# Kernel optimization log

Hardware: AMD Instinct MI355X
Metric: run time of the kernel (lower is better)

## Reference

```python
import jax, jax.numpy as jnp
import numpy as np

N = 4096
F = 256
E = 65536
NEG = -1e30  # mask value for non-neighbors in distance top-k


def setup_inputs() -> dict:
    key = jax.random.key(0)
    k1, k2, k3, k4, k5 = jax.random.split(key, 5)
    edge_index = jax.random.randint(k1, (2, E), 0, N)
    edge_weight = jax.random.uniform(k2, (E,), dtype=jnp.float32)
    features = jax.random.normal(k3, (N, F), dtype=jnp.float32)
    theta_1 = jax.random.uniform(k4, (1,), dtype=jnp.float32)
    theta_2 = jax.random.uniform(k5, (1,), dtype=jnp.float32)
    return {"edge_index": edge_index, "edge_weight": edge_weight,
            "features": features, "theta_1": theta_1, "theta_2": theta_2}


def reference(edge_index, edge_weight, features, theta_1, theta_2):
    n = features.shape[0]
    row, col = edge_index[0], edge_index[1]
    # Adjacency construction is done on detached numpy in the original.
    w = jax.lax.stop_gradient(edge_weight)
    X = jax.lax.stop_gradient(features)
    # sp.csr_matrix sums duplicate (i,j) entries -> scatter-add; + I; clamp >1 to 1
    A = jnp.zeros((n, n), jnp.float32).at[row, col].add(w)
    A = A + jnp.eye(n, dtype=jnp.float32)
    A = jnp.where(A > 1.0, 1.0, A)
    A2 = A @ A  # adjs[1] = sp_A ** 2
    # generate_sparse_ids mutates both A and A_robust(=A2 for r=2) with setdiag(0)
    off = 1.0 - jnp.eye(n, dtype=jnp.float32)
    A = A * off
    A2 = A2 * off
    D = jnp.sum(A != 0.0, axis=1)    # per-node degree (count_nonzero)
    Dr = jnp.sum(A2 != 0.0, axis=1)  # robust (2-hop) degree
    Df = D.astype(jnp.float32)
    d_thres = jnp.mean(Df) + 2.0 * jnp.std(Df)  # euclidean metric branch
    # squared-euclidean distances via gram trick: ||xu - xv||^2
    sq = jnp.sum(X * X, axis=1)
    dist2 = sq[:, None] + sq[None, :] - 2.0 * (X @ X.T)
    nbr2 = A2 != 0.0  # A_robust neighbors (diag excluded, already zeroed)
    dmask = jnp.where(nbr2, dist2, NEG)
    # rank of each candidate in descending-distance order (stable argsort)
    order = jnp.argsort(-dmask, axis=1)
    rank = jnp.argsort(order, axis=1)
    # nz_sel = D_r[u] - round(sparse_rate * D[u]) with sparse_rate=2.0 (exact ints)
    nz_sel = Dr - 2 * D
    # faithful to numpy argsort()[-0:] which selects ALL neighbors when nz_sel==0
    nz_eff = jnp.where(nz_sel == 0, n, nz_sel)
    Z_sparse = nbr2 & (rank < nz_eff[:, None])  # top nz_sel farthest neighbors
    Z_high = A == 0.0  # highD branch: zero all non-1-hop-neighbors
    highD = Df > d_thres
    nosparse = (~highD) & (2 * D > Dr)  # empty sparse_ids branch
    Z = jnp.where(highD[:, None], Z_high,
                  jnp.where(nosparse[:, None], False, Z_sparse))
    adj_k = jnp.where(Z, 0.0, A2 - A)  # diag already zero in both
    vals = theta_1 * edge_weight + theta_2 * jax.lax.stop_gradient(adj_k[row, col])
    return jnp.clip(vals, 0.0, None)
```

## Files before the change

### kernel.cpp

```cpp
#include <hip/hip_runtime.h>

#define NN 4096
#define FF 256
#define EE 65536
#define MAXDEG 128
#define MAXEPR 512
#define NCAND 2048

__device__ __forceinline__ float wred_max(float v) {
#pragma unroll
    for (int o = 32; o >= 1; o >>= 1) v = fmaxf(v, __shfl_xor(v, o));
    return v;
}
__device__ __forceinline__ int wred_sum(int v) {
#pragma unroll
    for (int o = 32; o >= 1; o >>= 1) v += __shfl_xor(v, o);
    return v;
}

__global__ void k_scatter(const int* __restrict__ ei, const float* __restrict__ ew,
                          float* __restrict__ A, int* __restrict__ ecnt,
                          int* __restrict__ elist) {
    int e = blockIdx.x * blockDim.x + threadIdx.x;
    if (e >= EE) return;
    int r = ei[e];
    int c = ei[EE + e];
    float w = ew[e];
    atomicAdd(&A[(size_t)r * NN + c], w);
    int p = atomicAdd(&ecnt[r], 1);
    if (p < MAXEPR) elist[r * MAXEPR + p] = e;
}

__global__ void k_csr(float* __restrict__ A, unsigned short* __restrict__ ccol,
                      float* __restrict__ cval, int* __restrict__ deg) {
    int wave = threadIdx.x >> 6;
    int lane = threadIdx.x & 63;
    int row = blockIdx.x * (blockDim.x >> 6) + wave;
    if (row >= NN) return;
    size_t base = (size_t)row * NN;
    unsigned long long lmask = (1ull << lane) - 1ull;
    int cnt = 0;
    for (int b = 0; b < NN; b += 256) {
        int c0 = b + lane * 4;
        float4 v = ((float4*)(A + base))[b / 4 + lane];
        v.x = (c0 + 0 == row) ? 0.f : fminf(v.x, 1.f);
        v.y = (c0 + 1 == row) ? 0.f : fminf(v.y, 1.f);
        v.z = (c0 + 2 == row) ? 0.f : fminf(v.z, 1.f);
        v.w = (c0 + 3 == row) ? 0.f : fminf(v.w, 1.f);
        ((float4*)(A + base))[b / 4 + lane] = v;
        float e[4] = {v.x, v.y, v.z, v.w};
#pragma unroll
        for (int j = 0; j < 4; ++j) {
            unsigned long long m = __ballot(e[j] != 0.f);
            int pos = cnt + __popcll(m & lmask);
            if (e[j] != 0.f && pos < MAXDEG) {
                ccol[row * MAXDEG + pos] = (unsigned short)(c0 + j);
                cval[row * MAXDEG + pos] = e[j];
            }
            cnt += __popcll(m);
        }
    }
    if (lane == 0) deg[row] = cnt;
}

__global__ void k_sq(const float* __restrict__ X, double* __restrict__ sq) {
    int wave = threadIdx.x >> 6;
    int lane = threadIdx.x & 63;
    int row = blockIdx.x * (blockDim.x >> 6) + wave;
    if (row >= NN) return;
    float4 x4 = ((const float4*)(X + (size_t)row * FF))[lane];
    double s = (double)x4.x * x4.x + (double)x4.y * x4.y +
               (double)x4.z * x4.z + (double)x4.w * x4.w;
#pragma unroll
    for (int o = 32; o >= 1; o >>= 1) s += __shfl_xor(s, o);
    if (lane == 0) sq[row] = s;
}

__global__ void k_stats(const int* __restrict__ deg, double* __restrict__ thres) {
    __shared__ double sd[256], sd2[256];
    int t = threadIdx.x;
    double s = 0, s2 = 0;
    for (int i = t; i < NN; i += 256) {
        double d = (double)deg[i];
        s += d; s2 += d * d;
    }
    sd[t] = s; sd2[t] = s2;
    __syncthreads();
    for (int o = 128; o >= 1; o >>= 1) {
        if (t < o) { sd[t] += sd[t + o]; sd2[t] += sd2[t + o]; }
        __syncthreads();
    }
    if (t == 0) {
        double mean = sd[0] / NN;
        double var = sd2[0] / NN - mean * mean;
        if (var < 0) var = 0;
        thres[0] = mean + 2.0 * sqrt(var);
    }
}

__launch_bounds__(256, 5)
__global__ void k_main(const int* __restrict__ ei, const float* __restrict__ ew,
                       const float* __restrict__ X, const float* __restrict__ th1p,
                       const float* __restrict__ th2p, const float* __restrict__ A,
                       const unsigned short* __restrict__ ccol,
                       const float* __restrict__ cval, const int* __restrict__ deg,
                       const int* __restrict__ ecnt, const int* __restrict__ elist,
                       const double* __restrict__ sq, const double* __restrict__ thresp,
                       float* __restrict__ out) {
    __shared__ float acc[NN];
    __shared__ float Xu[FF];
    __shared__ unsigned short cidx[NCAND];
    __shared__ float cdist[NCAND];
    __shared__ int ncand;

    const int u = blockIdx.x;
    const int tid = threadIdx.x;
    const int lane = tid & 63;
    const int wave = tid >> 6;
    const unsigned long long lmask = (1ull << lane) - 1ull;

    for (int i = tid; i < NN; i += 256) acc[i] = 0.f;
    if (tid < FF / 4)
        ((float4*)Xu)[tid] = ((const float4*)(X + (size_t)u * FF))[tid];
    if (tid == 0) ncand = 0;
    __syncthreads();

    const int du = deg[u];
    const int dul = min(du, MAXDEG);
    for (int kk = wave; kk <= dul; kk += 4) {
        int k; float wuk;
        if (kk == dul) { k = u; wuk = 1.f; }
        else { k = ccol[u * MAXDEG + kk]; wuk = cval[u * MAXDEG + kk]; }
        int dkl = min(deg[k], MAXDEG);
        for (int j = lane; j <= dkl; j += 64) {
            int v; float wkv;
            if (j == dkl) { v = k; wkv = 1.f; }
            else { v = ccol[k * MAXDEG + j]; wkv = cval[k * MAXDEG + j]; }
            atomicAdd(&acc[v], wuk * wkv);
        }
    }
    __syncthreads();
    if (tid == 0) acc[u] = 0.f;
    __syncthreads();

    for (int i = tid; i < NN; i += 256) {
        bool nz = (acc[i] != 0.f);
        unsigned long long m = __ballot(nz);
        int base = 0;
        if (lane == 0 && m) base = atomicAdd(&ncand, __popcll(m));
        base = __shfl(base, 0);
        int pos = base + __popcll(m & lmask);
        if (nz && pos < NCAND) cidx[pos] = (unsigned short)i;
    }
    __syncthreads();
    const int Dr = ncand;
    const int Drs = min(Dr, NCAND);

    const double squ = sq[u];
    for (int c = tid; c < Drs; c += 256) {
        int v = cidx[c];
        const float4* Xv = (const float4*)(X + (size_t)v * FF);
        double s0 = 0.0, s1 = 0.0;
#pragma unroll 4
        for (int f = 0; f < FF / 4; f += 2) {
            float4 a = Xv[f];
            float4 b = ((const float4*)Xu)[f];
            s0 += (double)a.x * b.x + (double)a.y * b.y +
                  (double)a.z * b.z + (double)a.w * b.w;
            float4 p = Xv[f + 1];
            float4 q = ((const float4*)Xu)[f + 1];
            s1 += (double)p.x * q.x + (double)p.y * q.y +
                  (double)p.z * q.z + (double)p.w * q.w;
        }
        cdist[c] = (float)(squ + sq[v] - 2.0 * (s0 + s1));
    }
    __syncthreads();

    const int D = du;
    const bool highD = ((double)D > thresp[0]);
    const int nz = Dr - 2 * D;
    const float th1 = th1p[0], th2 = th2p[0];
    int ne = ecnt[u]; if (ne > MAXEPR) ne = MAXEPR;
    for (int idx = wave; idx < ne; idx += 4) {
        int e = elist[u * MAXEPR + idx];
        int v = ei[EE + e];
        float w = ew[e];
        float a2v = acc[v];
        float av = A[(size_t)u * NN + v];
        float adj;
        if (highD) {
            adj = (av != 0.f) ? (a2v - av) : 0.f;
        } else if (nz < 0) {
            adj = a2v - av;
        } else if (nz == 0) {
            adj = 0.f;
        } else if (a2v == 0.f) {
            adj = 0.f;
        } else {
            float dvl = -3.4e38f;
            for (int c = lane; c < Drs; c += 64)
                if ((int)cidx[c] == v) dvl = cdist[c];
            float dv = wred_max(dvl);
            int cnt = 0;
            for (int c = lane; c < Drs; c += 64) {
                float cd = cdist[c];
                int ci = cidx[c];
                cnt += (cd > dv || (cd == dv && ci < v)) ? 1 : 0;
            }
            cnt = wred_sum(cnt);
            adj = (cnt < nz) ? 0.f : (a2v - av);
        }
        if (lane == 0) out[e] = fmaxf(0.f, fmaf(th1, w, th2 * adj));
    }
}

extern "C" void kernel_launch(void* const* d_in, const int* in_sizes, int n_in,
                              void* d_out, int out_size, void* d_ws, size_t ws_size,
                              hipStream_t stream) {
    const int* ei = (const int*)d_in[0];
    const float* ew = (const float*)d_in[1];
    const float* X = (const float*)d_in[2];
    const float* th1 = (const float*)d_in[3];
    const float* th2 = (const float*)d_in[4];
    float* out = (float*)d_out;

    char* ws = (char*)d_ws;
    size_t off = 0;
    float* A = (float*)(ws + off);            off += (size_t)NN * NN * 4;
    unsigned short* ccol = (unsigned short*)(ws + off); off += (size_t)NN * MAXDEG * 2;
    float* cval = (float*)(ws + off);         off += (size_t)NN * MAXDEG * 4;
    int* deg = (int*)(ws + off);              off += (size_t)NN * 4;
    int* elist = (int*)(ws + off);            off += (size_t)NN * MAXEPR * 4;
    int* ecnt = (int*)(ws + off);             off += (size_t)NN * 4;
    double* sq = (double*)(ws + off);         off += (size_t)NN * 8;
    double* thres = (double*)(ws + off);      off += 256;

    hipMemsetAsync(A, 0, (size_t)NN * NN * 4, stream);
    hipMemsetAsync(ecnt, 0, (size_t)NN * 4, stream);

    k_scatter<<<EE / 256, 256, 0, stream>>>(ei, ew, A, ecnt, elist);
    k_csr<<<NN / 4, 256, 0, stream>>>(A, ccol, cval, deg);
    k_sq<<<NN / 4, 256, 0, stream>>>(X, sq);
    k_stats<<<1, 256, 0, stream>>>(deg, thres);
    k_main<<<NN, 256, 0, stream>>>(ei, ew, X, th1, th2, A, ccol, cval, deg,
                                   ecnt, elist, sq, thres, out);
}
```

Before: 308.2 us.

## Build sparse adjacency directly from edge lists, dropping dense NxN matrix

Replaces the dense N×N adjacency scatter, memset and row scan with a per-row wave that dedups edges via shuffles and builds the CSR lists directly, fused with the squared-norm computation. The main kernel caches the row's neighbor list in shared memory and looks up A[u,v] there instead of reading the dense matrix. Distance dot products are split across 4 lanes per candidate for coalesced feature loads. This removes large dense-matrix memory traffic, at the cost of O(64) shuffle loops per edge chunk and a linear shared-memory search.

```diff
diff --git a/kernel.cpp b/kernel.cpp
--- a/kernel.cpp
+++ b/kernel.cpp
@@ -6,74 +6,85 @@
 #define MAXDEG 128
 #define MAXEPR 512
 #define NCAND 2048
-
-__device__ __forceinline__ float wred_max(float v) {
-#pragma unroll
-    for (int o = 32; o >= 1; o >>= 1) v = fmaxf(v, __shfl_xor(v, o));
-    return v;
-}
+#define LLEN 160
+
 __device__ __forceinline__ int wred_sum(int v) {
 #pragma unroll
     for (int o = 32; o >= 1; o >>= 1) v += __shfl_xor(v, o);
     return v;
 }
 
-__global__ void k_scatter(const int* __restrict__ ei, const float* __restrict__ ew,
-                          float* __restrict__ A, int* __restrict__ ecnt,
+__global__ void k_scatter(const int* __restrict__ ei, int* __restrict__ ecnt,
                           int* __restrict__ elist) {
     int e = blockIdx.x * blockDim.x + threadIdx.x;
     if (e >= EE) return;
     int r = ei[e];
-    int c = ei[EE + e];
-    float w = ew[e];
-    atomicAdd(&A[(size_t)r * NN + c], w);
     int p = atomicAdd(&ecnt[r], 1);
     if (p < MAXEPR) elist[r * MAXEPR + p] = e;
 }
 
-__global__ void k_csr(float* __restrict__ A, unsigned short* __restrict__ ccol,
-                      float* __restrict__ cval, int* __restrict__ deg) {
-    int wave = threadIdx.x >> 6;
-    int lane = threadIdx.x & 63;
-    int row = blockIdx.x * (blockDim.x >> 6) + wave;
-    if (row >= NN) return;
-    size_t base = (size_t)row * NN;
-    unsigned long long lmask = (1ull << lane) - 1ull;
-    int cnt = 0;
-    for (int b = 0; b < NN; b += 256) {
-        int c0 = b + lane * 4;
-        float4 v = ((float4*)(A + base))[b / 4 + lane];
-        v.x = (c0 + 0 == row) ? 0.f : fminf(v.x, 1.f);
-        v.y = (c0 + 1 == row) ? 0.f : fminf(v.y, 1.f);
-        v.z = (c0 + 2 == row) ? 0.f : fminf(v.z, 1.f);
-        v.w = (c0 + 3 == row) ? 0.f : fminf(v.w, 1.f);
-        ((float4*)(A + base))[b / 4 + lane] = v;
-        float e[4] = {v.x, v.y, v.z, v.w};
-#pragma unroll
-        for (int j = 0; j < 4; ++j) {
-            unsigned long long m = __ballot(e[j] != 0.f);
-            int pos = cnt + __popcll(m & lmask);
-            if (e[j] != 0.f && pos < MAXDEG) {
-                ccol[row * MAXDEG + pos] = (unsigned short)(c0 + j);
-                cval[row * MAXDEG + pos] = e[j];
+__global__ void k_build(const int* __restrict__ ei, const float* __restrict__ ew,
+                        const int* __restrict__ ecnt, const int* __restrict__ elist,
+                        const float* __restrict__ X,
+                        unsigned short* __restrict__ ccol, float* __restrict__ cval,
+                        int* __restrict__ deg, double* __restrict__ sq) {
+    __shared__ unsigned short lcol[4][LLEN];
+    __shared__ float lval[4][LLEN];
+    const int wv = threadIdx.x >> 6;
+    const int lane = threadIdx.x & 63;
+    const int u = blockIdx.x * 4 + wv;
+    if (u >= NN) return;
+    const unsigned long long lmask = (1ull << lane) - 1ull;
+
+    int ne = ecnt[u]; if (ne > MAXEPR) ne = MAXEPR;
+    int len = 0;
+    for (int base = 0; base < ne; base += 64) {
+        int i = base + lane;
+        bool act = (i < ne);
+        int e = act ? elist[u * MAXEPR + i] : 0;
+        int c = act ? ei[EE + e] : -1;
+        if (c == u) { act = false; c = -1; }
+        float w = act ? ew[e] : 0.f;
+        float sum = 0.f;
+        bool leader = act;
+        for (int j = 0; j < 64; ++j) {
+            int cj = __shfl(c, j);
+            float wj = __shfl(w, j);
+            if (act && cj == c) {
+                sum += wj;
+                if (j < lane) leader = false;
             }
-            cnt += __popcll(m);
-        }
-    }
-    if (lane == 0) deg[row] = cnt;
-}
-
-__global__ void k_sq(const float* __restrict__ X, double* __restrict__ sq) {
-    int wave = threadIdx.x >> 6;
-    int lane = threadIdx.x & 63;
-    int row = blockIdx.x * (blockDim.x >> 6) + wave;
-    if (row >= NN) return;
-    float4 x4 = ((const float4*)(X + (size_t)row * FF))[lane];
+        }
+        if (base == 0) {
+            unsigned long long m = __ballot(leader);
+            int pos = __popcll(m & lmask);
+            if (leader && pos < LLEN) { lcol[wv][pos] = (unsigned short)c; lval[wv][pos] = sum; }
+            len = __popcll(m);
+        } else {
+            int found = -1;
+            if (leader) {
+                for (int t = 0; t < len; ++t)
+                    if ((int)lcol[wv][t] == c) { found = t; break; }
+            }
+            if (leader && found >= 0) lval[wv][found] += sum;
+            unsigned long long m = __ballot(leader && found < 0);
+            int pos = len + __popcll(m & lmask);
+            if (leader && found < 0 && pos < LLEN) { lcol[wv][pos] = (unsigned short)c; lval[wv][pos] = sum; }
+            len += __popcll(m);
+        }
+    }
+    for (int t = lane; t < len && t < MAXDEG; t += 64) {
+        ccol[u * MAXDEG + t] = lcol[wv][t];
+        cval[u * MAXDEG + t] = fminf(lval[wv][t], 1.f);
+    }
+    if (lane == 0) deg[u] = len;
+
+    float4 x4 = ((const float4*)(X + (size_t)u * FF))[lane];
     double s = (double)x4.x * x4.x + (double)x4.y * x4.y +
                (double)x4.z * x4.z + (double)x4.w * x4.w;
 #pragma unroll
     for (int o = 32; o >= 1; o >>= 1) s += __shfl_xor(s, o);
-    if (lane == 0) sq[row] = s;
+    if (lane == 0) sq[u] = s;
 }
 
 __global__ void k_stats(const int* __restrict__ deg, double* __restrict__ thres) {
@@ -101,7 +112,7 @@
 __launch_bounds__(256, 5)
 __global__ void k_main(const int* __restrict__ ei, const float* __restrict__ ew,
                        const float* __restrict__ X, const float* __restrict__ th1p,
-                       const float* __restrict__ th2p, const float* __restrict__ A,
+                       const float* __restrict__ th2p,
                        const unsigned short* __restrict__ ccol,
                        const float* __restrict__ cval, const int* __restrict__ deg,
                        const int* __restrict__ ecnt, const int* __restrict__ elist,
@@ -111,6 +122,8 @@
     __shared__ float Xu[FF];
     __shared__ unsigned short cidx[NCAND];
     __shared__ float cdist[NCAND];
+    __shared__ unsigned short Aucol[MAXDEG];
+    __shared__ float Auval[MAXDEG];
     __shared__ int ncand;
 
     const int u = blockIdx.x;
@@ -119,18 +132,22 @@
     const int wave = tid >> 6;
     const unsigned long long lmask = (1ull << lane) - 1ull;
 
+    const int du = deg[u];
+    const int dul = min(du, MAXDEG);
     for (int i = tid; i < NN; i += 256) acc[i] = 0.f;
     if (tid < FF / 4)
         ((float4*)Xu)[tid] = ((const float4*)(X + (size_t)u * FF))[tid];
+    if (tid >= 128 && tid - 128 < dul) {
+        Aucol[tid - 128] = ccol[u * MAXDEG + tid - 128];
+        Auval[tid - 128] = cval[u * MAXDEG + tid - 128];
+    }
     if (tid == 0) ncand = 0;
     __syncthreads();
 
-    const int du = deg[u];
-    const int dul = min(du, MAXDEG);
     for (int kk = wave; kk <= dul; kk += 4) {
         int k; float wuk;
         if (kk == dul) { k = u; wuk = 1.f; }
-        else { k = ccol[u * MAXDEG + kk]; wuk = cval[u * MAXDEG + kk]; }
+        else { k = Aucol[kk]; wuk = Auval[kk]; }
         int dkl = min(deg[k], MAXDEG);
         for (int j = lane; j <= dkl; j += 64) {
             int v; float wkv;
@@ -144,35 +161,37 @@
     __syncthreads();
 
     for (int i = tid; i < NN; i += 256) {
-        bool nz = (acc[i] != 0.f);
-        unsigned long long m = __ballot(nz);
+        bool nzf = (acc[i] != 0.f);
+        unsigned long long m = __ballot(nzf);
         int base = 0;
         if (lane == 0 && m) base = atomicAdd(&ncand, __popcll(m));
         base = __shfl(base, 0);
         int pos = base + __popcll(m & lmask);
-        if (nz && pos < NCAND) cidx[pos] = (unsigned short)i;
+        if (nzf && pos < NCAND) cidx[pos] = (unsigned short)i;
     }
     __syncthreads();
     const int Dr = ncand;
     const int Drs = min(Dr, NCAND);
 
     const double squ = sq[u];
-    for (int c = tid; c < Drs; c += 256) {
-        int v = cidx[c];
+    const int sub = lane & 3;
+    for (int c0 = wave * 16; c0 < Drs; c0 += 64) {
+        int ci = c0 + (lane >> 2);
+        bool live = (ci < Drs);
+        int v = live ? cidx[ci] : 0;
         const float4* Xv = (const float4*)(X + (size_t)v * FF);
-        double s0 = 0.0, s1 = 0.0;
-#pragma unroll 4
-        for (int f = 0; f < FF / 4; f += 2) {
-            float4 a = Xv[f];
-            float4 b = ((const float4*)Xu)[f];
-            s0 += (double)a.x * b.x + (double)a.y * b.y +
-                  (double)a.z * b.z + (double)a.w * b.w;
-            float4 p = Xv[f + 1];
-            float4 q = ((const float4*)Xu)[f + 1];
-            s1 += (double)p.x * q.x + (double)p.y * q.y +
-                  (double)p.z * q.z + (double)p.w * q.w;
-        }
-        cdist[c] = (float)(squ + sq[v] - 2.0 * (s0 + s1));
+        double s = 0.0;
+#pragma unroll
+        for (int i = 0; i < 16; ++i) {
+            float4 a = Xv[i * 4 + sub];
+            float4 b = ((const float4*)Xu)[i * 4 + sub];
+            s += (double)a.x * b.x + (double)a.y * b.y +
+                 (double)a.z * b.z + (double)a.w * b.w;
+        }
+        s += __shfl_xor(s, 1);
+        s += __shfl_xor(s, 2);
+        if (live && sub == 0)
+            cdist[ci] = (float)(squ + sq[v] - 2.0 * s);
     }
     __syncthreads();
 
@@ -186,7 +205,12 @@
         int v = ei[EE + e];
         float w = ew[e];
         float a2v = acc[v];
-        float av = A[(size_t)u * NN + v];
+        float avl = 0.f;
+        bool hit = false;
+        for (int t = lane; t < dul; t += 64)
+            if ((int)Aucol[t] == v) { avl = Auval[t]; hit = true; }
+        unsigned long long hm = __ballot(hit);
+        float av = hm ? __shfl(avl, (int)__builtin_ctzll(hm)) : 0.f;
         float adj;
         if (highD) {
             adj = (av != 0.f) ? (a2v - av) : 0.f;
@@ -197,10 +221,11 @@
         } else if (a2v == 0.f) {
             adj = 0.f;
         } else {
-            float dvl = -3.4e38f;
+            float dvl = 0.f; bool fnd = false;
             for (int c = lane; c < Drs; c += 64)
-                if ((int)cidx[c] == v) dvl = cdist[c];
-            float dv = wred_max(dvl);
+                if ((int)cidx[c] == v) { dvl = cdist[c]; fnd = true; }
+            unsigned long long fm = __ballot(fnd);
+            float dv = __shfl(dvl, (int)__builtin_ctzll(fm));
             int cnt = 0;
             for (int c = lane; c < Drs; c += 64) {
                 float cd = cdist[c];
@@ -226,7 +251,6 @@
 
     char* ws = (char*)d_ws;
     size_t off = 0;
-    float* A = (float*)(ws + off);            off += (size_t)NN * NN * 4;
     unsigned short* ccol = (unsigned short*)(ws + off); off += (size_t)NN * MAXDEG * 2;
     float* cval = (float*)(ws + off);         off += (size_t)NN * MAXDEG * 4;
     int* deg = (int*)(ws + off);              off += (size_t)NN * 4;
@@ -235,13 +259,11 @@
     double* sq = (double*)(ws + off);         off += (size_t)NN * 8;
     double* thres = (double*)(ws + off);      off += 256;
 
-    hipMemsetAsync(A, 0, (size_t)NN * NN * 4, stream);
     hipMemsetAsync(ecnt, 0, (size_t)NN * 4, stream);
 
-    k_scatter<<<EE / 256, 256, 0, stream>>>(ei, ew, A, ecnt, elist);
-    k_csr<<<NN / 4, 256, 0, stream>>>(A, ccol, cval, deg);
-    k_sq<<<NN / 4, 256, 0, stream>>>(X, sq);
+    k_scatter<<<EE / 256, 256, 0, stream>>>(ei, ecnt, elist);
+    k_build<<<NN / 4, 256, 0, stream>>>(ei, ew, ecnt, elist, X, ccol, cval, deg, sq);
     k_stats<<<1, 256, 0, stream>>>(deg, thres);
-    k_main<<<NN, 256, 0, stream>>>(ei, ew, X, th1, th2, A, ccol, cval, deg,
+    k_main<<<NN, 256, 0, stream>>>(ei, ew, X, th1, th2, ccol, cval, deg,
                                    ecnt, elist, sq, thres, out);
 }
```

Result: slower. 449.7 us (+45.9%).
